# Kernel optimization log

Measured on AMD Instinct MI355X. Metric: run time of the kernel, lower is better.

Reference implementation:

```python
import jax, jax.numpy as jnp
import numpy as np

B, S, D, H = 2, 2048, 1024, 16
HD = D // H  # 64


def setup_inputs() -> dict:
    key = jax.random.key(0)
    ks = jax.random.split(key, 7)
    s = 1.0 / np.sqrt(HD)
    return {
        "x": jax.random.normal(ks[0], (B, S, D), dtype=jnp.float32),
        "Wq": jax.random.normal(ks[1], (H, HD, HD), dtype=jnp.float32) * s,
        "bq": jax.random.normal(ks[2], (H, HD), dtype=jnp.float32) * 0.01,
        "Wk": jax.random.normal(ks[3], (H, HD, HD), dtype=jnp.float32) * s,
        "bk": jax.random.normal(ks[4], (H, HD), dtype=jnp.float32) * 0.01,
        "Wv": jax.random.normal(ks[5], (H, HD, HD), dtype=jnp.float32) * s,
        "bv": jax.random.normal(ks[6], (H, HD), dtype=jnp.float32) * 0.01,
    }


def reference(x, Wq, bq, Wk, bk, Wv, bv):
    b, s, d = x.shape
    h, hd, _ = Wq.shape
    # Faithful to torch: x.view(B, H, S, hd) is a raw reshape (mixes seq positions
    # across heads), NOT a transpose-based head split.
    xh = x.reshape(b, h, s, hd)
    # torch Linear: y @ W.T + b, with W of shape (out, in)
    q = jnp.einsum('bhse,hde->bhsd', xh, Wq) + bq[None, :, None, :]
    k = jnp.einsum('bhse,hde->bhsd', xh, Wk) + bk[None, :, None, :]
    v = jnp.einsum('bhse,hde->bhsd', xh, Wv) + bv[None, :, None, :]
    scale = 1.0 / jnp.sqrt(jnp.asarray(d / h, dtype=jnp.float32))
    attn = jax.nn.softmax(jnp.einsum('bhqd,bhkd->bhqk', q, k) * scale, axis=-1)
    out = jnp.einsum('bhqk,bhkd->bhqd', attn, v)
    # torch.cat over heads along last dim == transpose then merge
    return out.transpose(0, 2, 1, 3).reshape(b, s, d)
```

## Files before the change

kernel.cpp:

```cpp
#include <hip/hip_runtime.h>
#include <hip/hip_bf16.h>

#define BATCH 2
#define SEQ   2048
#define DMODEL 1024
#define NH    16
#define HD    64
#define QSCALE 0.1803368801111602f

typedef __attribute__((ext_vector_type(8))) short bf16x8;
typedef __attribute__((ext_vector_type(4))) float f32x4;

__device__ __forceinline__ ushort f2bf(float f) {
    union { float f; unsigned u; } v; v.f = f;
    return (ushort)((v.u + 0x8000u) >> 16);
}

__device__ __forceinline__ unsigned pack2bf(float a, float b) {
    union { float f; unsigned u; } x, y; x.f = a; y.f = b;
    return __builtin_amdgcn_perm(y.u + 0x8000u, x.u + 0x8000u, 0x07060302u);
}

__device__ __forceinline__ float exp2r(float x) {
#if __has_builtin(__builtin_amdgcn_exp2f)
    return __builtin_amdgcn_exp2f(x);
#else
    return exp2f(x);
#endif
}

#define MFMA(a, b, c) __builtin_amdgcn_mfma_f32_16x16x32_bf16((a), (b), (c), 0, 0, 0)

__global__ __launch_bounds__(256) void qkv_kernel(
    const float* __restrict__ x,
    const float* __restrict__ Wq, const float* __restrict__ bq,
    const float* __restrict__ Wk, const float* __restrict__ bk,
    const float* __restrict__ bv, const float* __restrict__ Wv,
    ushort* __restrict__ Qo, ushort* __restrict__ Kf, ushort* __restrict__ Vf)
{
    const int bid = blockIdx.x;
    const int st  = bid & 31;
    const int bh  = bid >> 5;
    const int h   = bh & (NH - 1);

    __shared__ ushort Xs[64 * 72];
    __shared__ ushort Ws[3 * 64 * 72];

    const int tid  = threadIdx.x;
    const int wave = tid >> 6, lane = tid & 63;
    const int ln16 = lane & 15, quad = lane >> 4;

    const float* xp = x + (size_t)bh * (SEQ * HD) + (size_t)st * 64 * HD;
    for (int i = 0; i < 4; ++i) {
        int idx = tid + 256 * i;
        float4 v = ((const float4*)xp)[idx];
        int row = idx >> 4, c4 = (idx & 15) * 4;
        ushort4 o;
        o.x = f2bf(v.x); o.y = f2bf(v.y); o.z = f2bf(v.z); o.w = f2bf(v.w);
        *(ushort4*)&Xs[row * 72 + c4] = o;
    }
    const float* wsrc[3] = { Wq + h * 4096, Wk + h * 4096, Wv + h * 4096 };
    for (int m = 0; m < 3; ++m)
        for (int i = 0; i < 4; ++i) {
            int idx = tid + 256 * i;
            float4 v = ((const float4*)wsrc[m])[idx];
            if (m == 0) { v.x *= QSCALE; v.y *= QSCALE; v.z *= QSCALE; v.w *= QSCALE; }
            int row = idx >> 4, c4 = (idx & 15) * 4;
            ushort4 o;
            o.x = f2bf(v.x); o.y = f2bf(v.y); o.z = f2bf(v.z); o.w = f2bf(v.w);
            *(ushort4*)&Ws[m * 64 * 72 + row * 72 + c4] = o;
        }
    __syncthreads();

    bf16x8 afr[2];
    for (int ks = 0; ks < 2; ++ks)
        afr[ks] = *(const bf16x8*)&Xs[(wave * 16 + ln16) * 72 + ks * 32 + quad * 8];
    __syncthreads();

    ushort* Eb = Xs;
    const float* bias[3] = { bq + h * 64, bk + h * 64, bv + h * 64 };

    for (int m = 0; m < 3; ++m) {
        f32x4 acc[4];
        for (int nt = 0; nt < 4; ++nt) {
            acc[nt] = (f32x4){0.f, 0.f, 0.f, 0.f};
            for (int ks = 0; ks < 2; ++ks) {
                bf16x8 bfr = *(const bf16x8*)&Ws[m * 64 * 72 + (nt * 16 + ln16) * 72 + ks * 32 + quad * 8];
                acc[nt] = MFMA(afr[ks], bfr, acc[nt]);
            }
        }
        if (m < 2) {
            for (int nt = 0; nt < 4; ++nt) {
                float bb = bias[m][nt * 16 + ln16];
                if (m == 0) bb *= QSCALE;
                for (int r = 0; r < 4; ++r)
                    Eb[(wave * 16 + quad * 4 + r) * 72 + nt * 16 + ln16] = f2bf(acc[nt][r] + bb);
            }
            __syncthreads();
            if (m == 0) {
                ushort* dst = Qo + (size_t)bh * SEQ * HD + (size_t)st * 64 * HD;
                for (int i = 0; i < 2; ++i) {
                    int idx = tid + 256 * i;
                    int row = idx >> 3, c8 = (idx & 7) * 8;
                    *(bf16x8*)&dst[row * 64 + c8] = *(const bf16x8*)&Eb[row * 72 + c8];
                }
            } else {
                ushort* dst = Kf + ((size_t)bh * 32 + st) * 4096;
                for (int i = 0; i < 2; ++i) {
                    int idx8 = tid + 256 * i;
                    int l2 = idx8 & 63, chunk = idx8 >> 6;
                    int nt = chunk >> 1, ks = chunk & 1;
                    int qd = l2 >> 4, l16 = l2 & 15;
                    *(bf16x8*)&dst[(size_t)idx8 * 8] =
                        *(const bf16x8*)&Eb[(nt * 16 + l16) * 72 + ks * 32 + qd * 8];
                }
            }
            __syncthreads();
        } else {
            for (int nt = 0; nt < 4; ++nt) {
                float bb = bias[2][nt * 16 + ln16];
                ushort4 o;
                o.x = f2bf(acc[nt][0] + bb);
                o.y = f2bf(acc[nt][1] + bb);
                o.z = f2bf(acc[nt][2] + bb);
                o.w = f2bf(acc[nt][3] + bb);
                *(ushort4*)&Eb[(nt * 16 + ln16) * 72 + wave * 16 + quad * 4] = o;
            }
            __syncthreads();
            ushort* dst = Vf + ((size_t)bh * 32 + st) * 4096;
            for (int i = 0; i < 2; ++i) {
                int idx8 = tid + 256 * i;
                int l2 = idx8 & 63, chunk = idx8 >> 6;
                int nt = chunk >> 1, ks = chunk & 1;
                int qd = l2 >> 4, l16 = l2 & 15;
                *(bf16x8*)&dst[(size_t)idx8 * 8] =
                    *(const bf16x8*)&Eb[(nt * 16 + l16) * 72 + ks * 32 + qd * 8];
            }
        }
    }
}

__global__ __launch_bounds__(256, 2) void attn_kernel(
    const ushort* __restrict__ Q, const ushort* __restrict__ Kf,
    const ushort* __restrict__ Vf, float* __restrict__ out)
{
    const int bid = blockIdx.x;
    const int qt  = bid & 15;
    const int bh  = bid >> 4;
    const int h   = bh & (NH - 1), b = bh >> 4;

    __shared__ ushort Ps[4][32 * 72];

    const int tid = threadIdx.x, wave = tid >> 6, lane = tid & 63;
    const int ln16 = lane & 15, quad = lane >> 4;

    bf16x8 qfr[2][2];
#pragma unroll
    for (int g = 0; g < 2; ++g) {
        const ushort* Qg = Q + ((size_t)bh * SEQ + qt * 128 + wave * 32 + g * 16 + ln16) * HD;
        qfr[g][0] = *(const bf16x8*)&Qg[quad * 8];
        qfr[g][1] = *(const bf16x8*)&Qg[32 + quad * 8];
    }

    const bf16x8* kfp = (const bf16x8*)(Kf + (size_t)bh * 32 * 4096) + lane;
    const bf16x8* vfp = (const bf16x8*)(Vf + (size_t)bh * 32 * 4096) + lane;

    float lsum[2] = {0.f, 0.f};
    f32x4 accO[2][4];
#pragma unroll
    for (int g = 0; g < 2; ++g)
#pragma unroll
        for (int nt = 0; nt < 4; ++nt) accO[g][nt] = (f32x4){0.f, 0.f, 0.f, 0.f};

    ushort* Pw = Ps[wave];

    bf16x8 kf[8];
#pragma unroll
    for (int c = 0; c < 8; ++c) kf[c] = kfp[c * 64];
    kfp += 512;

    for (int kt = 0; kt < 32; ++kt) {
        f32x4 sacc[2][4];
#pragma unroll
        for (int nt = 0; nt < 4; ++nt)
#pragma unroll
            for (int g = 0; g < 2; ++g) {
                f32x4 a = {0.f, 0.f, 0.f, 0.f};
                a = MFMA(kf[nt * 2],     qfr[g][0], a);
                a = MFMA(kf[nt * 2 + 1], qfr[g][1], a);
                sacc[g][nt] = a;
            }

        bf16x8 vf[8];
#pragma unroll
        for (int c = 0; c < 8; ++c) vf[c] = vfp[c * 64];
        vfp += 512;
        if (kt < 31) {
#pragma unroll
            for (int c = 0; c < 8; ++c) kf[c] = kfp[c * 64];
            kfp += 512;
        }

#pragma unroll
        for (int g = 0; g < 2; ++g) {
            float rs = 0.f;
#pragma unroll
            for (int nt = 0; nt < 4; ++nt) {
                float p0 = exp2r(sacc[g][nt][0]);
                float p1 = exp2r(sacc[g][nt][1]);
                float p2 = exp2r(sacc[g][nt][2]);
                float p3 = exp2r(sacc[g][nt][3]);
                rs += (p0 + p1) + (p2 + p3);
                uint2 pk;
                pk.x = pack2bf(p0, p1);
                pk.y = pack2bf(p2, p3);
                *(uint2*)&Pw[(g * 16 + ln16) * 72 + nt * 16 + quad * 4] = pk;
            }
            lsum[g] += rs;
        }

        bf16x8 pf[2][2];
#pragma unroll
        for (int g = 0; g < 2; ++g) {
            pf[g][0] = *(const bf16x8*)&Pw[(g * 16 + ln16) * 72 + quad * 8];
            pf[g][1] = *(const bf16x8*)&Pw[(g * 16 + ln16) * 72 + 32 + quad * 8];
        }

#pragma unroll
        for (int nt = 0; nt < 4; ++nt)
#pragma unroll
            for (int g = 0; g < 2; ++g) {
                accO[g][nt] = MFMA(vf[nt * 2],     pf[g][0], accO[g][nt]);
                accO[g][nt] = MFMA(vf[nt * 2 + 1], pf[g][1], accO[g][nt]);
            }
    }

#pragma unroll
    for (int g = 0; g < 2; ++g) {
        float l = lsum[g];
        l += __shfl_xor(l, 16, 64);
        l += __shfl_xor(l, 32, 64);
        float rinv = 1.0f / l;
        float* ob = out + ((size_t)b * SEQ + qt * 128 + wave * 32 + g * 16 + ln16) * DMODEL + h * HD;
#pragma unroll
        for (int nt = 0; nt < 4; ++nt) {
            float4 o;
            o.x = accO[g][nt][0] * rinv;
            o.y = accO[g][nt][1] * rinv;
            o.z = accO[g][nt][2] * rinv;
            o.w = accO[g][nt][3] * rinv;
            *(float4*)&ob[nt * 16 + quad * 4] = o;
        }
    }
}

extern "C" void kernel_launch(void* const* d_in, const int* in_sizes, int n_in,
                              void* d_out, int out_size, void* d_ws, size_t ws_size,
                              hipStream_t stream) {
    const float* x  = (const float*)d_in[0];
    const float* Wq = (const float*)d_in[1];
    const float* bq = (const float*)d_in[2];
    const float* Wk = (const float*)d_in[3];
    const float* bk = (const float*)d_in[4];
    const float* Wv = (const float*)d_in[5];
    const float* bv = (const float*)d_in[6];

    const size_t nElem = (size_t)BATCH * NH * SEQ * HD;
    ushort* Qw = (ushort*)d_ws;
    ushort* Kw = Qw + nElem;
    ushort* Vw = Kw + nElem;

    qkv_kernel<<<BATCH * NH * (SEQ / 64), 256, 0, stream>>>(
        x, Wq, bq, Wk, bk, bv, Wv, Qw, Kw, Vw);
    attn_kernel<<<BATCH * NH * (SEQ / 128), 256, 0, stream>>>(
        Qw, Kw, Vw, (float*)d_out);
}
```

Measured before the change: 136.5 us.

## Pipeline PV MFMA with next-tile softmax and batch QKV tiles per block

```diff
diff --git a/kernel.cpp b/kernel.cpp
--- a/kernel.cpp
+++ b/kernel.cpp
@@ -35,12 +35,12 @@
     const float* __restrict__ x,
     const float* __restrict__ Wq, const float* __restrict__ bq,
     const float* __restrict__ Wk, const float* __restrict__ bk,
-    const float* __restrict__ bv, const float* __restrict__ Wv,
+    const float* __restrict__ Wv, const float* __restrict__ bv,
     ushort* __restrict__ Qo, ushort* __restrict__ Kf, ushort* __restrict__ Vf)
 {
     const int bid = blockIdx.x;
-    const int st  = bid & 31;
-    const int bh  = bid >> 5;
+    const int ch  = bid & 7;
+    const int bh  = bid >> 3;
     const int h   = bh & (NH - 1);
 
     __shared__ ushort Xs[64 * 72];
@@ -50,15 +50,6 @@
     const int wave = tid >> 6, lane = tid & 63;
     const int ln16 = lane & 15, quad = lane >> 4;
 
-    const float* xp = x + (size_t)bh * (SEQ * HD) + (size_t)st * 64 * HD;
-    for (int i = 0; i < 4; ++i) {
-        int idx = tid + 256 * i;
-        float4 v = ((const float4*)xp)[idx];
-        int row = idx >> 4, c4 = (idx & 15) * 4;
-        ushort4 o;
-        o.x = f2bf(v.x); o.y = f2bf(v.y); o.z = f2bf(v.z); o.w = f2bf(v.w);
-        *(ushort4*)&Xs[row * 72 + c4] = o;
-    }
     const float* wsrc[3] = { Wq + h * 4096, Wk + h * 4096, Wv + h * 4096 };
     for (int m = 0; m < 3; ++m)
         for (int i = 0; i < 4; ++i) {
@@ -70,42 +61,78 @@
             o.x = f2bf(v.x); o.y = f2bf(v.y); o.z = f2bf(v.z); o.w = f2bf(v.w);
             *(ushort4*)&Ws[m * 64 * 72 + row * 72 + c4] = o;
         }
-    __syncthreads();
-
-    bf16x8 afr[2];
-    for (int ks = 0; ks < 2; ++ks)
-        afr[ks] = *(const bf16x8*)&Xs[(wave * 16 + ln16) * 72 + ks * 32 + quad * 8];
-    __syncthreads();
-
+
+    const float* bias[3] = { bq + h * 64, bk + h * 64, bv + h * 64 };
     ushort* Eb = Xs;
-    const float* bias[3] = { bq + h * 64, bk + h * 64, bv + h * 64 };
-
-    for (int m = 0; m < 3; ++m) {
-        f32x4 acc[4];
-        for (int nt = 0; nt < 4; ++nt) {
-            acc[nt] = (f32x4){0.f, 0.f, 0.f, 0.f};
-            for (int ks = 0; ks < 2; ++ks) {
-                bf16x8 bfr = *(const bf16x8*)&Ws[m * 64 * 72 + (nt * 16 + ln16) * 72 + ks * 32 + quad * 8];
-                acc[nt] = MFMA(afr[ks], bfr, acc[nt]);
-            }
-        }
-        if (m < 2) {
+
+    for (int tt = 0; tt < 4; ++tt) {
+        const int st = ch * 4 + tt;
+        __syncthreads();
+
+        const float* xp = x + (size_t)bh * (SEQ * HD) + (size_t)st * 64 * HD;
+        for (int i = 0; i < 4; ++i) {
+            int idx = tid + 256 * i;
+            float4 v = ((const float4*)xp)[idx];
+            int row = idx >> 4, c4 = (idx & 15) * 4;
+            ushort4 o;
+            o.x = f2bf(v.x); o.y = f2bf(v.y); o.z = f2bf(v.z); o.w = f2bf(v.w);
+            *(ushort4*)&Xs[row * 72 + c4] = o;
+        }
+        __syncthreads();
+
+        bf16x8 afr[2];
+        for (int ks = 0; ks < 2; ++ks)
+            afr[ks] = *(const bf16x8*)&Xs[(wave * 16 + ln16) * 72 + ks * 32 + quad * 8];
+        __syncthreads();
+
+        for (int m = 0; m < 3; ++m) {
+            f32x4 acc[4];
             for (int nt = 0; nt < 4; ++nt) {
-                float bb = bias[m][nt * 16 + ln16];
-                if (m == 0) bb *= QSCALE;
-                for (int r = 0; r < 4; ++r)
-                    Eb[(wave * 16 + quad * 4 + r) * 72 + nt * 16 + ln16] = f2bf(acc[nt][r] + bb);
-            }
-            __syncthreads();
-            if (m == 0) {
-                ushort* dst = Qo + (size_t)bh * SEQ * HD + (size_t)st * 64 * HD;
-                for (int i = 0; i < 2; ++i) {
-                    int idx = tid + 256 * i;
-                    int row = idx >> 3, c8 = (idx & 7) * 8;
-                    *(bf16x8*)&dst[row * 64 + c8] = *(const bf16x8*)&Eb[row * 72 + c8];
-                }
+                acc[nt] = (f32x4){0.f, 0.f, 0.f, 0.f};
+                for (int ks = 0; ks < 2; ++ks) {
+                    bf16x8 bfr = *(const bf16x8*)&Ws[m * 64 * 72 + (nt * 16 + ln16) * 72 + ks * 32 + quad * 8];
+                    acc[nt] = MFMA(afr[ks], bfr, acc[nt]);
+                }
+            }
+            if (m < 2) {
+                for (int nt = 0; nt < 4; ++nt) {
+                    float bb = bias[m][nt * 16 + ln16];
+                    if (m == 0) bb *= QSCALE;
+                    for (int r = 0; r < 4; ++r)
+                        Eb[(wave * 16 + quad * 4 + r) * 72 + nt * 16 + ln16] = f2bf(acc[nt][r] + bb);
+                }
+                __syncthreads();
+                if (m == 0) {
+                    ushort* dst = Qo + (size_t)bh * SEQ * HD + (size_t)st * 64 * HD;
+                    for (int i = 0; i < 2; ++i) {
+                        int idx = tid + 256 * i;
+                        int row = idx >> 3, c8 = (idx & 7) * 8;
+                        *(bf16x8*)&dst[row * 64 + c8] = *(const bf16x8*)&Eb[row * 72 + c8];
+                    }
+                } else {
+                    ushort* dst = Kf + ((size_t)bh * 32 + st) * 4096;
+                    for (int i = 0; i < 2; ++i) {
+                        int idx8 = tid + 256 * i;
+                        int l2 = idx8 & 63, chunk = idx8 >> 6;
+                        int nt = chunk >> 1, ks = chunk & 1;
+                        int qd = l2 >> 4, l16 = l2 & 15;
+                        *(bf16x8*)&dst[(size_t)idx8 * 8] =
+                            *(const bf16x8*)&Eb[(nt * 16 + l16) * 72 + ks * 32 + qd * 8];
+                    }
+                }
+                __syncthreads();
             } else {
-                ushort* dst = Kf + ((size_t)bh * 32 + st) * 4096;
+                for (int nt = 0; nt < 4; ++nt) {
+                    float bb = bias[2][nt * 16 + ln16];
+                    ushort4 o;
+                    o.x = f2bf(acc[nt][0] + bb);
+                    o.y = f2bf(acc[nt][1] + bb);
+                    o.z = f2bf(acc[nt][2] + bb);
+                    o.w = f2bf(acc[nt][3] + bb);
+                    *(ushort4*)&Eb[(nt * 16 + ln16) * 72 + wave * 16 + quad * 4] = o;
+                }
+                __syncthreads();
+                ushort* dst = Vf + ((size_t)bh * 32 + st) * 4096;
                 for (int i = 0; i < 2; ++i) {
                     int idx8 = tid + 256 * i;
                     int l2 = idx8 & 63, chunk = idx8 >> 6;
@@ -114,27 +141,6 @@
                     *(bf16x8*)&dst[(size_t)idx8 * 8] =
                         *(const bf16x8*)&Eb[(nt * 16 + l16) * 72 + ks * 32 + qd * 8];
                 }
-            }
-            __syncthreads();
-        } else {
-            for (int nt = 0; nt < 4; ++nt) {
-                float bb = bias[2][nt * 16 + ln16];
-                ushort4 o;
-                o.x = f2bf(acc[nt][0] + bb);
-                o.y = f2bf(acc[nt][1] + bb);
-                o.z = f2bf(acc[nt][2] + bb);
-                o.w = f2bf(acc[nt][3] + bb);
-                *(ushort4*)&Eb[(nt * 16 + ln16) * 72 + wave * 16 + quad * 4] = o;
-            }
-            __syncthreads();
-            ushort* dst = Vf + ((size_t)bh * 32 + st) * 4096;
-            for (int i = 0; i < 2; ++i) {
-                int idx8 = tid + 256 * i;
-                int l2 = idx8 & 63, chunk = idx8 >> 6;
-                int nt = chunk >> 1, ks = chunk & 1;
-                int qd = l2 >> 4, l16 = l2 & 15;
-                *(bf16x8*)&dst[(size_t)idx8 * 8] =
-                    *(const bf16x8*)&Eb[(nt * 16 + l16) * 72 + ks * 32 + qd * 8];
             }
         }
     }
@@ -149,7 +155,7 @@
     const int bh  = bid >> 4;
     const int h   = bh & (NH - 1), b = bh >> 4;
 
-    __shared__ ushort Ps[4][32 * 72];
+    __shared__ ushort Ps[4][2][32 * 72];
 
     const int tid = threadIdx.x, wave = tid >> 6, lane = tid & 63;
     const int ln16 = lane & 15, quad = lane >> 4;
@@ -172,14 +178,14 @@
 #pragma unroll
         for (int nt = 0; nt < 4; ++nt) accO[g][nt] = (f32x4){0.f, 0.f, 0.f, 0.f};
 
-    ushort* Pw = Ps[wave];
-
-    bf16x8 kf[8];
+    bf16x8 kf[8], vf[8];
 #pragma unroll
     for (int c = 0; c < 8; ++c) kf[c] = kfp[c * 64];
     kfp += 512;
 
     for (int kt = 0; kt < 32; ++kt) {
+        const int cur = kt & 1;
+
         f32x4 sacc[2][4];
 #pragma unroll
         for (int nt = 0; nt < 4; ++nt)
@@ -191,16 +197,34 @@
                 sacc[g][nt] = a;
             }
 
-        bf16x8 vf[8];
+        if (kt < 31) {
+#pragma unroll
+            for (int c = 0; c < 8; ++c) kf[c] = kfp[c * 64];
+            kfp += 512;
+        }
+
+        if (kt > 0) {
+            const ushort* Pr = Ps[wave][1 - cur];
+            bf16x8 pf[2][2];
+#pragma unroll
+            for (int g = 0; g < 2; ++g) {
+                pf[g][0] = *(const bf16x8*)&Pr[(g * 16 + ln16) * 72 + quad * 8];
+                pf[g][1] = *(const bf16x8*)&Pr[(g * 16 + ln16) * 72 + 32 + quad * 8];
+            }
+#pragma unroll
+            for (int nt = 0; nt < 4; ++nt)
+#pragma unroll
+                for (int g = 0; g < 2; ++g) {
+                    accO[g][nt] = MFMA(vf[nt * 2],     pf[g][0], accO[g][nt]);
+                    accO[g][nt] = MFMA(vf[nt * 2 + 1], pf[g][1], accO[g][nt]);
+                }
+        }
+
 #pragma unroll
         for (int c = 0; c < 8; ++c) vf[c] = vfp[c * 64];
         vfp += 512;
-        if (kt < 31) {
-#pragma unroll
-            for (int c = 0; c < 8; ++c) kf[c] = kfp[c * 64];
-            kfp += 512;
-        }
-
+
+        ushort* Pw = Ps[wave][cur];
 #pragma unroll
         for (int g = 0; g < 2; ++g) {
             float rs = 0.f;
@@ -218,14 +242,16 @@
             }
             lsum[g] += rs;
         }
-
+    }
+
+    {
+        const ushort* Pr = Ps[wave][31 & 1];
         bf16x8 pf[2][2];
 #pragma unroll
         for (int g = 0; g < 2; ++g) {
-            pf[g][0] = *(const bf16x8*)&Pw[(g * 16 + ln16) * 72 + quad * 8];
-            pf[g][1] = *(const bf16x8*)&Pw[(g * 16 + ln16) * 72 + 32 + quad * 8];
-        }
-
+            pf[g][0] = *(const bf16x8*)&Pr[(g * 16 + ln16) * 72 + quad * 8];
+            pf[g][1] = *(const bf16x8*)&Pr[(g * 16 + ln16) * 72 + 32 + quad * 8];
+        }
 #pragma unroll
         for (int nt = 0; nt < 4; ++nt)
 #pragma unroll
@@ -270,8 +296,8 @@
     ushort* Kw = Qw + nElem;
     ushort* Vw = Kw + nElem;
 
-    qkv_kernel<<<BATCH * NH * (SEQ / 64), 256, 0, stream>>>(
-        x, Wq, bq, Wk, bk, bv, Wv, Qw, Kw, Vw);
+    qkv_kernel<<<32 * 8, 256, 0, stream>>>(
+        x, Wq, bq, Wk, bk, Wv, bv, Qw, Kw, Vw);
     attn_kernel<<<BATCH * NH * (SEQ / 128), 256, 0, stream>>>(
         Qw, Kw, Vw, (float*)d_out);
 }
```

Result: faster. 128.4 us (-6.0%).
